# Kernel optimization log

Measured on AMD Instinct MI355X. Metric: run time of the kernel, lower is better.

## Reference

```python
import jax, jax.numpy as jnp
import numpy as np

N_NODES = 50000
N_EDGES = 600000
D = 128


def setup_inputs() -> dict:
    key = jax.random.key(0)
    k = jax.random.split(key, 6)
    x = jax.random.normal(k[0], (N_NODES, D), dtype=jnp.float32)
    edge_src = jax.random.randint(k[1], (N_EDGES,), 0, N_NODES, dtype=jnp.int64 if jax.config.jax_enable_x64 else jnp.int32)
    edge_dst = jax.random.randint(k[2], (N_EDGES,), 0, N_NODES, dtype=jnp.int64 if jax.config.jax_enable_x64 else jnp.int32)
    # message MLP: [h_src ; h_dst] (2D) -> D, update MLP: [h ; agg] (2D) -> D
    scale = 1.0 / np.sqrt(2 * D)
    W1 = jax.random.normal(k[3], (2 * D, D), dtype=jnp.float32) * scale
    b1 = jnp.zeros((D,), dtype=jnp.float32)
    W2 = jax.random.normal(k[4], (2 * D, D), dtype=jnp.float32) * scale
    b2 = jnp.zeros((D,), dtype=jnp.float32)
    return {"x": x, "edge_src": edge_src, "edge_dst": edge_dst,
            "W1": W1, "b1": b1, "W2": W2, "b2": b2}


def reference(x, edge_src, edge_dst, W1, b1, W2, b2):
    # gather endpoint features per edge: [E, 2D]
    pair = jnp.concatenate([x[edge_src], x[edge_dst]], axis=-1)
    # per-edge message MLP: [E, D]
    msg = jax.nn.relu(pair @ W1 + b1)
    # scatter-aggregate (sum) messages into destination nodes: [N, D]
    agg = jax.ops.segment_sum(msg, edge_dst, num_segments=N_NODES)
    # node update MLP with residual: [N, D]
    upd = jax.nn.relu(jnp.concatenate([x, agg], axis=-1) @ W2 + b2)
    return x + upd
```

## Files before the change

kernel.cpp:

```cpp
#include <hip/hip_runtime.h>
#include <stdint.h>


typedef __attribute__((ext_vector_type(8))) short short8;
typedef __attribute__((ext_vector_type(4))) float floatx4;

#define D 128

static __device__ __forceinline__ unsigned short f2bf(float f) {
    union { float f; unsigned int u; } v; v.f = f;
    unsigned int r = (v.u + 0x7fffu + ((v.u >> 16) & 1u)) >> 16;
    return (unsigned short)r;
}
static __device__ __forceinline__ float bflo(unsigned int u) {
    union { unsigned int u; float f; } v; v.u = u << 16; return v.f;
}
static __device__ __forceinline__ float bfhi(unsigned int u) {
    union { unsigned int u; float f; } v; v.u = u & 0xffff0000u; return v.f;
}

__global__ void k_convert_w(const float* __restrict__ W1, const float* __restrict__ W2,
                            unsigned short* __restrict__ w1f, unsigned short* __restrict__ w2f,
                            int* __restrict__ cursor, int N) {
    int gid = blockIdx.x * blockDim.x + threadIdx.x;
    if (gid < N) cursor[gid] = 0;
    if (gid < 32768) {
        int tid = gid;
        int j = tid & 7, lane = (tid >> 3) & 63, ct = (tid >> 9) & 15, kk = tid >> 13;
        int k = kk * 32 + (lane >> 4) * 8 + j;
        int c = ((ct >> 2) << 6) + ((lane & 15) << 2) + (ct & 3);
        float v = (c < 128) ? W1[k * 128 + c] : W1[(128 + k) * 128 + (c - 128)];
        w1f[tid] = f2bf(v);
    } else {
        int tid = gid - 32768;
        int j = tid & 7, lane = (tid >> 3) & 63, ct = (tid >> 9) & 7, kk = tid >> 12;
        int k = kk * 32 + (lane >> 4) * 8 + j;
        int c = ((ct >> 1) << 5) + ((lane & 15) << 1) + (ct & 1);
        w2f[tid] = f2bf(W2[k * 128 + c]);
    }
}

__global__ __launch_bounds__(256) void k_gemm1(
    const float* __restrict__ x,
    const unsigned short* __restrict__ w1f,
    const float* __restrict__ b1,
    unsigned short* __restrict__ xb,
    unsigned short* __restrict__ Ys,
    unsigned short* __restrict__ Yd,
    int N, int nTiles)
{
    const int tid = threadIdx.x, w = tid >> 6, lane = tid & 63;
    const int quad = lane >> 4, col = lane & 15;

    short8 wf[4][4];
#pragma unroll
    for (int kk = 0; kk < 4; kk++)
#pragma unroll
        for (int j = 0; j < 4; j++)
            wf[kk][j] = ((const short8*)w1f)[(kk * 16 + w * 4 + j) * 64 + lane];
    float4 bias = make_float4(0.f, 0.f, 0.f, 0.f);
    if (w >= 2) bias = *(const float4*)(b1 + (w - 2) * 64 + col * 4);
    unsigned short* Yhalf = (w < 2) ? Ys : Yd;
    const int cb = (w & 1) * 64;

    for (int t = blockIdx.x; t < nTiles; t += gridDim.x) {
        const int n0 = t * 16;
        const int nr = n0 + col;
        const float* xrow = x + (long)nr * D;
        floatx4 acc[4];
#pragma unroll
        for (int j = 0; j < 4; j++)
#pragma unroll
            for (int q = 0; q < 4; q++) acc[j][q] = 0.f;
#pragma unroll
        for (int kk = 0; kk < 4; kk++) {
            float4 f0 = *(const float4*)(xrow + kk * 32 + quad * 8);
            float4 f1 = *(const float4*)(xrow + kk * 32 + quad * 8 + 4);
            union { short8 s; unsigned int u[4]; } au;
            asm("v_cvt_pk_bf16_f32 %0, %1, %2" : "=v"(au.u[0]) : "v"(f0.x), "v"(f0.y));
            asm("v_cvt_pk_bf16_f32 %0, %1, %2" : "=v"(au.u[1]) : "v"(f0.z), "v"(f0.w));
            asm("v_cvt_pk_bf16_f32 %0, %1, %2" : "=v"(au.u[2]) : "v"(f1.x), "v"(f1.y));
            asm("v_cvt_pk_bf16_f32 %0, %1, %2" : "=v"(au.u[3]) : "v"(f1.z), "v"(f1.w));
            if (w == 0)
                *(short8*)(xb + (long)nr * D + kk * 32 + quad * 8) = au.s;
#pragma unroll
            for (int j = 0; j < 4; j++)
                acc[j] = __builtin_amdgcn_mfma_f32_16x16x32_bf16(au.s, wf[kk][j], acc[j], 0, 0, 0);
        }
#pragma unroll
        for (int r = 0; r < 4; r++) {
            int n = n0 + quad * 4 + r;
            ushort4 o;
            o.x = f2bf(acc[0][r] + bias.x);
            o.y = f2bf(acc[1][r] + bias.y);
            o.z = f2bf(acc[2][r] + bias.z);
            o.w = f2bf(acc[3][r] + bias.w);
            *(ushort4*)(Yhalf + (long)n * D + cb + col * 4) = o;
        }
    }
}

__global__ void k_hist(const int* __restrict__ dst, int* __restrict__ cnt, int E) {
    int i = blockIdx.x * blockDim.x + threadIdx.x;
    if (i < E) atomicAdd(&cnt[dst[i]], 1);
}

__global__ void k_scanA(const int* __restrict__ cnt, int* __restrict__ rowptr,
                        int* __restrict__ bsum, int N) {
    __shared__ int ws[16];
    int tid = threadIdx.x, i = blockIdx.x * 1024 + tid;
    int lane = tid & 63, wv = tid >> 6;
    int c = (i < N) ? cnt[i] : 0;
    int incl = c;
#pragma unroll
    for (int off = 1; off < 64; off <<= 1) {
        int t = __shfl_up(incl, off, 64);
        if (lane >= off) incl += t;
    }
    if (lane == 63) ws[wv] = incl;
    __syncthreads();
    if (wv == 0) {
        int v = (lane < 16) ? ws[lane] : 0;
        int s = v;
#pragma unroll
        for (int off = 1; off < 16; off <<= 1) {
            int t = __shfl_up(s, off, 64);
            if (lane >= off) s += t;
        }
        if (lane < 16) ws[lane] = s - v;
    }
    __syncthreads();
    if (i < N) rowptr[i] = incl - c + ws[wv];
    if (tid == 1023) bsum[blockIdx.x] = ws[15] + incl;
}

__global__ void k_scanC(int* __restrict__ rowptr, int* __restrict__ cursor,
                        const int* __restrict__ bsum, int N, int E, int nb) {
    __shared__ int off_s;
    int tid = threadIdx.x;
    int chunk = blockIdx.x >> 2;
    if (tid < 64) {
        int v = (tid < chunk && tid < nb) ? bsum[tid] : 0;
#pragma unroll
        for (int off = 32; off; off >>= 1) v += __shfl_down(v, off, 64);
        if (tid == 0) off_s = v;
    }
    __syncthreads();
    int i = blockIdx.x * 256 + tid;
    if (i < N) {
        int r = rowptr[i] + off_s;
        rowptr[i] = r;
        cursor[i] = r;
    }
    if (i == 0) rowptr[N] = E;
}

__global__ void k_scatter(const int* __restrict__ src, const int* __restrict__ dst,
                          int* __restrict__ cursor, int* __restrict__ ssrc, int E) {
    int i = blockIdx.x * blockDim.x + threadIdx.x;
    if (i < E) {
        int p = atomicAdd(&cursor[dst[i]], 1);
        ssrc[p] = src[i];
    }
}

__global__ __launch_bounds__(256) void k_agg(
    const unsigned short* __restrict__ Ys,
    const unsigned short* __restrict__ Yd,
    const int* __restrict__ rowptr,
    const int* __restrict__ ssrc,
    unsigned short* __restrict__ aggb, int N)
{
    int wv = blockIdx.x * 4 + (threadIdx.x >> 6);
    if (wv >= N) return;
    int lane = threadIdx.x & 63;
    int rp0 = rowptr[wv], rp1 = rowptr[wv + 1];
    unsigned int ydu = *(const unsigned int*)(Yd + (long)wv * D + lane * 2);
    float yd0 = bflo(ydu), yd1 = bfhi(ydu);
    float a0 = 0.f, a1 = 0.f;
    const unsigned short* ysl = Ys + lane * 2;
    int e = rp0;
    for (; e + 8 <= rp1; e += 8) {
        int s[8]; unsigned int u[8];
#pragma unroll
        for (int q = 0; q < 8; q++) s[q] = ssrc[e + q];
#pragma unroll
        for (int q = 0; q < 8; q++) u[q] = *(const unsigned int*)(ysl + (long)s[q] * D);
#pragma unroll
        for (int q = 0; q < 8; q++) {
            a0 += fmaxf(bflo(u[q]) + yd0, 0.f);
            a1 += fmaxf(bfhi(u[q]) + yd1, 0.f);
        }
    }
    for (; e + 4 <= rp1; e += 4) {
        int s[4]; unsigned int u[4];
#pragma unroll
        for (int q = 0; q < 4; q++) s[q] = ssrc[e + q];
#pragma unroll
        for (int q = 0; q < 4; q++) u[q] = *(const unsigned int*)(ysl + (long)s[q] * D);
#pragma unroll
        for (int q = 0; q < 4; q++) {
            a0 += fmaxf(bflo(u[q]) + yd0, 0.f);
            a1 += fmaxf(bfhi(u[q]) + yd1, 0.f);
        }
    }
    for (; e < rp1; e++) {
        unsigned int u0 = *(const unsigned int*)(ysl + (long)ssrc[e] * D);
        a0 += fmaxf(bflo(u0) + yd0, 0.f);
        a1 += fmaxf(bfhi(u0) + yd1, 0.f);
    }
    unsigned int o = (unsigned int)f2bf(a0) | ((unsigned int)f2bf(a1) << 16);
    *(unsigned int*)(aggb + (long)wv * D + lane * 2) = o;
}

__global__ __launch_bounds__(256) void k_gemm2(
    const unsigned short* __restrict__ xb,
    const unsigned short* __restrict__ aggb,
    const unsigned short* __restrict__ w2f,
    const float* __restrict__ b2,
    const float* __restrict__ x,
    float* __restrict__ out,
    int N, int nTiles)
{
    const int tid = threadIdx.x, w = tid >> 6, lane = tid & 63;
    const int quad = lane >> 4, col = lane & 15;

    short8 wf[8][2];
#pragma unroll
    for (int kk = 0; kk < 8; kk++)
#pragma unroll
        for (int c = 0; c < 2; c++)
            wf[kk][c] = ((const short8*)w2f)[(kk * 8 + w * 2 + c) * 64 + lane];
    float2 bias = *(const float2*)(b2 + w * 32 + col * 2);

    for (int t = blockIdx.x; t < nTiles; t += gridDim.x) {
        const int n0 = t * 16;
        const int nr = n0 + col;
        floatx4 acc[2];
#pragma unroll
        for (int c = 0; c < 2; c++)
#pragma unroll
            for (int q = 0; q < 4; q++) acc[c][q] = 0.f;
#pragma unroll
        for (int kk = 0; kk < 8; kk++) {
            const unsigned short* base = (kk < 4) ? xb : aggb;
            short8 a = *(const short8*)(base + (long)nr * D + (kk & 3) * 32 + quad * 8);
            acc[0] = __builtin_amdgcn_mfma_f32_16x16x32_bf16(a, wf[kk][0], acc[0], 0, 0, 0);
            acc[1] = __builtin_amdgcn_mfma_f32_16x16x32_bf16(a, wf[kk][1], acc[1], 0, 0, 0);
        }
#pragma unroll
        for (int r = 0; r < 4; r++) {
            int n = n0 + quad * 4 + r;
            long off = (long)n * D + w * 32 + col * 2;
            float2 xr = *(const float2*)(x + off);
            float v0 = fmaxf(acc[0][r] + bias.x, 0.f);
            float v1 = fmaxf(acc[1][r] + bias.y, 0.f);
            *(float2*)(out + off) = make_float2(xr.x + v0, xr.y + v1);
        }
    }
}

extern "C" void kernel_launch(void* const* d_in, const int* in_sizes, int n_in,
                              void* d_out, int out_size, void* d_ws, size_t ws_size,
                              hipStream_t stream)
{
    const float* x   = (const float*)d_in[0];
    const int* esrc  = (const int*)d_in[1];
    const int* edst  = (const int*)d_in[2];
    const float* W1  = (const float*)d_in[3];
    const float* b1  = (const float*)d_in[4];
    const float* W2  = (const float*)d_in[5];
    const float* b2  = (const float*)d_in[6];
    float* out = (float*)d_out;

    const int ND = in_sizes[0];
    const int N  = ND / D;
    const int E  = in_sizes[1];

    char* p = (char*)d_ws;
    auto alloc = [&](size_t bytes) { char* r = p; p += (bytes + 255) & ~(size_t)255; return r; };
    unsigned short* Ys   = (unsigned short*)alloc((size_t)ND * 2);
    unsigned short* Yd   = (unsigned short*)alloc((size_t)ND * 2);
    unsigned short* xb   = (unsigned short*)alloc((size_t)ND * 2);
    unsigned short* aggb = (unsigned short*)alloc((size_t)ND * 2);
    unsigned short* w1f  = (unsigned short*)alloc(32768 * 2);
    unsigned short* w2f  = (unsigned short*)alloc(32768 * 2);
    int* rowptr = (int*)alloc((size_t)(N + 1) * 4);
    int* cursor = (int*)alloc((size_t)N * 4);
    int* bsum   = (int*)alloc(64 * 4);
    int* ssrc   = (int*)alloc((size_t)E * 4);

    const int nTiles = N / 16;
    const int nb = (N + 1023) / 1024;

    k_convert_w<<<256, 256, 0, stream>>>(W1, W2, w1f, w2f, cursor, N);
    k_gemm1<<<1024, 256, 0, stream>>>(x, w1f, b1, xb, Ys, Yd, N, nTiles);
    k_hist<<<(E + 255) / 256, 256, 0, stream>>>(edst, cursor, E);
    k_scanA<<<nb, 1024, 0, stream>>>(cursor, rowptr, bsum, N);
    k_scanC<<<(N + 255) / 256, 256, 0, stream>>>(rowptr, cursor, bsum, N, E, nb);
    k_scatter<<<(E + 255) / 256, 256, 0, stream>>>(esrc, edst, cursor, ssrc, E);
    k_agg<<<(N + 3) / 4, 256, 0, stream>>>(Ys, Yd, rowptr, ssrc, aggb, N);
    k_gemm2<<<1024, 256, 0, stream>>>(xb, aggb, w2f, b2, x, out, N, nTiles);
}
```

Measured before the change: 211.9 us.

## Fuse all pipeline stages into one cooperative persistent kernel with grid syncs

Replaces the eight separate launches (weight conversion, GEMM1, histogram, two scan passes, scatter, aggregation, GEMM2) with one cooperative kernel that separates phases with grid.sync(). It also drops the bf16 copy of x: GEMM2 now reloads fp32 x and converts it in registers. The histogram is fused into the GEMM1 phase, and the scan is reworked to four elements per thread across 256-thread blocks. The aim is to remove per-launch overhead and inter-kernel gaps. The cost is grid-wide barriers, reduced occupancy because the grid is capped by cooperative residency, and the combined register pressure of all phases in one kernel.

Result: slower. 468.5 us (+121.1%).

```diff
diff --git a/kernel.cpp b/kernel.cpp
--- a/kernel.cpp
+++ b/kernel.cpp
@@ -1,5 +1,8 @@
 #include <hip/hip_runtime.h>
+#include <hip/hip_cooperative_groups.h>
 #include <stdint.h>
+
+namespace cg = cooperative_groups;
 
 
 typedef __attribute__((ext_vector_type(8))) short short8;
@@ -19,243 +22,260 @@
     union { unsigned int u; float f; } v; v.u = u & 0xffff0000u; return v.f;
 }
 
-__global__ void k_convert_w(const float* __restrict__ W1, const float* __restrict__ W2,
-                            unsigned short* __restrict__ w1f, unsigned short* __restrict__ w2f,
-                            int* __restrict__ cursor, int N) {
-    int gid = blockIdx.x * blockDim.x + threadIdx.x;
-    if (gid < N) cursor[gid] = 0;
-    if (gid < 32768) {
-        int tid = gid;
-        int j = tid & 7, lane = (tid >> 3) & 63, ct = (tid >> 9) & 15, kk = tid >> 13;
-        int k = kk * 32 + (lane >> 4) * 8 + j;
-        int c = ((ct >> 2) << 6) + ((lane & 15) << 2) + (ct & 3);
-        float v = (c < 128) ? W1[k * 128 + c] : W1[(128 + k) * 128 + (c - 128)];
-        w1f[tid] = f2bf(v);
-    } else {
-        int tid = gid - 32768;
-        int j = tid & 7, lane = (tid >> 3) & 63, ct = (tid >> 9) & 7, kk = tid >> 12;
-        int k = kk * 32 + (lane >> 4) * 8 + j;
-        int c = ((ct >> 1) << 5) + ((lane & 15) << 1) + (ct & 1);
-        w2f[tid] = f2bf(W2[k * 128 + c]);
-    }
-}
-
-__global__ __launch_bounds__(256) void k_gemm1(
+
+__global__ __launch_bounds__(256) void k_mega(
     const float* __restrict__ x,
-    const unsigned short* __restrict__ w1f,
+    const int* __restrict__ esrc,
+    const int* __restrict__ edst,
+    const float* __restrict__ W1,
     const float* __restrict__ b1,
-    unsigned short* __restrict__ xb,
+    const float* __restrict__ W2,
+    const float* __restrict__ b2,
+    float* __restrict__ out,
+    unsigned short* __restrict__ w1f,
+    unsigned short* __restrict__ w2f,
     unsigned short* __restrict__ Ys,
     unsigned short* __restrict__ Yd,
-    int N, int nTiles)
+    unsigned short* __restrict__ aggb,
+    int* __restrict__ cnt,
+    int* __restrict__ rowptr,
+    int* __restrict__ cursor,
+    int* __restrict__ bsum,
+    int* __restrict__ ssrc,
+    int N, int E, int nTiles)
 {
-    const int tid = threadIdx.x, w = tid >> 6, lane = tid & 63;
+    cg::grid_group grid = cg::this_grid();
+    const int G  = gridDim.x;
+    const int GT = G * 256;
+    const int tid = threadIdx.x;
+    const int gid0 = blockIdx.x * 256 + tid;
+    const int w = tid >> 6, lane = tid & 63;
     const int quad = lane >> 4, col = lane & 15;
-
-    short8 wf[4][4];
-#pragma unroll
-    for (int kk = 0; kk < 4; kk++)
-#pragma unroll
-        for (int j = 0; j < 4; j++)
-            wf[kk][j] = ((const short8*)w1f)[(kk * 16 + w * 4 + j) * 64 + lane];
-    float4 bias = make_float4(0.f, 0.f, 0.f, 0.f);
-    if (w >= 2) bias = *(const float4*)(b1 + (w - 2) * 64 + col * 4);
-    unsigned short* Yhalf = (w < 2) ? Ys : Yd;
-    const int cb = (w & 1) * 64;
-
-    for (int t = blockIdx.x; t < nTiles; t += gridDim.x) {
-        const int n0 = t * 16;
-        const int nr = n0 + col;
-        const float* xrow = x + (long)nr * D;
-        floatx4 acc[4];
-#pragma unroll
-        for (int j = 0; j < 4; j++)
-#pragma unroll
-            for (int q = 0; q < 4; q++) acc[j][q] = 0.f;
-#pragma unroll
-        for (int kk = 0; kk < 4; kk++) {
-            float4 f0 = *(const float4*)(xrow + kk * 32 + quad * 8);
-            float4 f1 = *(const float4*)(xrow + kk * 32 + quad * 8 + 4);
-            union { short8 s; unsigned int u[4]; } au;
-            asm("v_cvt_pk_bf16_f32 %0, %1, %2" : "=v"(au.u[0]) : "v"(f0.x), "v"(f0.y));
-            asm("v_cvt_pk_bf16_f32 %0, %1, %2" : "=v"(au.u[1]) : "v"(f0.z), "v"(f0.w));
-            asm("v_cvt_pk_bf16_f32 %0, %1, %2" : "=v"(au.u[2]) : "v"(f1.x), "v"(f1.y));
-            asm("v_cvt_pk_bf16_f32 %0, %1, %2" : "=v"(au.u[3]) : "v"(f1.z), "v"(f1.w));
-            if (w == 0)
-                *(short8*)(xb + (long)nr * D + kk * 32 + quad * 8) = au.s;
+    __shared__ int sh[9];
+
+    for (int i = gid0; i < N; i += GT) cnt[i] = 0;
+    for (int g = gid0; g < 65536; g += GT) {
+        if (g < 32768) {
+            int j = g & 7, l = (g >> 3) & 63, ct = (g >> 9) & 15, kk = g >> 13;
+            int k = kk * 32 + (l >> 4) * 8 + j;
+            int c = ((ct >> 2) << 6) + ((l & 15) << 2) + (ct & 3);
+            float v = (c < 128) ? W1[k * 128 + c] : W1[(128 + k) * 128 + (c - 128)];
+            w1f[g] = f2bf(v);
+        } else {
+            int t2 = g - 32768;
+            int j = t2 & 7, l = (t2 >> 3) & 63, ct = (t2 >> 9) & 7, kk = t2 >> 12;
+            int k = kk * 32 + (l >> 4) * 8 + j;
+            int c = ((ct >> 1) << 5) + ((l & 15) << 1) + (ct & 1);
+            w2f[t2] = f2bf(W2[k * 128 + c]);
+        }
+    }
+    grid.sync();
+
+    {
+        short8 wf[4][4];
+#pragma unroll
+        for (int kk = 0; kk < 4; kk++)
 #pragma unroll
             for (int j = 0; j < 4; j++)
-                acc[j] = __builtin_amdgcn_mfma_f32_16x16x32_bf16(au.s, wf[kk][j], acc[j], 0, 0, 0);
-        }
-#pragma unroll
-        for (int r = 0; r < 4; r++) {
-            int n = n0 + quad * 4 + r;
-            ushort4 o;
-            o.x = f2bf(acc[0][r] + bias.x);
-            o.y = f2bf(acc[1][r] + bias.y);
-            o.z = f2bf(acc[2][r] + bias.z);
-            o.w = f2bf(acc[3][r] + bias.w);
-            *(ushort4*)(Yhalf + (long)n * D + cb + col * 4) = o;
-        }
-    }
-}
-
-__global__ void k_hist(const int* __restrict__ dst, int* __restrict__ cnt, int E) {
-    int i = blockIdx.x * blockDim.x + threadIdx.x;
-    if (i < E) atomicAdd(&cnt[dst[i]], 1);
-}
-
-__global__ void k_scanA(const int* __restrict__ cnt, int* __restrict__ rowptr,
-                        int* __restrict__ bsum, int N) {
-    __shared__ int ws[16];
-    int tid = threadIdx.x, i = blockIdx.x * 1024 + tid;
-    int lane = tid & 63, wv = tid >> 6;
-    int c = (i < N) ? cnt[i] : 0;
-    int incl = c;
-#pragma unroll
-    for (int off = 1; off < 64; off <<= 1) {
-        int t = __shfl_up(incl, off, 64);
-        if (lane >= off) incl += t;
-    }
-    if (lane == 63) ws[wv] = incl;
-    __syncthreads();
-    if (wv == 0) {
-        int v = (lane < 16) ? ws[lane] : 0;
-        int s = v;
-#pragma unroll
-        for (int off = 1; off < 16; off <<= 1) {
-            int t = __shfl_up(s, off, 64);
-            if (lane >= off) s += t;
-        }
-        if (lane < 16) ws[lane] = s - v;
-    }
-    __syncthreads();
-    if (i < N) rowptr[i] = incl - c + ws[wv];
-    if (tid == 1023) bsum[blockIdx.x] = ws[15] + incl;
-}
-
-__global__ void k_scanC(int* __restrict__ rowptr, int* __restrict__ cursor,
-                        const int* __restrict__ bsum, int N, int E, int nb) {
-    __shared__ int off_s;
-    int tid = threadIdx.x;
-    int chunk = blockIdx.x >> 2;
-    if (tid < 64) {
-        int v = (tid < chunk && tid < nb) ? bsum[tid] : 0;
-#pragma unroll
-        for (int off = 32; off; off >>= 1) v += __shfl_down(v, off, 64);
-        if (tid == 0) off_s = v;
-    }
-    __syncthreads();
-    int i = blockIdx.x * 256 + tid;
-    if (i < N) {
-        int r = rowptr[i] + off_s;
-        rowptr[i] = r;
-        cursor[i] = r;
-    }
-    if (i == 0) rowptr[N] = E;
-}
-
-__global__ void k_scatter(const int* __restrict__ src, const int* __restrict__ dst,
-                          int* __restrict__ cursor, int* __restrict__ ssrc, int E) {
-    int i = blockIdx.x * blockDim.x + threadIdx.x;
-    if (i < E) {
-        int p = atomicAdd(&cursor[dst[i]], 1);
-        ssrc[p] = src[i];
-    }
-}
-
-__global__ __launch_bounds__(256) void k_agg(
-    const unsigned short* __restrict__ Ys,
-    const unsigned short* __restrict__ Yd,
-    const int* __restrict__ rowptr,
-    const int* __restrict__ ssrc,
-    unsigned short* __restrict__ aggb, int N)
-{
-    int wv = blockIdx.x * 4 + (threadIdx.x >> 6);
-    if (wv >= N) return;
-    int lane = threadIdx.x & 63;
-    int rp0 = rowptr[wv], rp1 = rowptr[wv + 1];
-    unsigned int ydu = *(const unsigned int*)(Yd + (long)wv * D + lane * 2);
-    float yd0 = bflo(ydu), yd1 = bfhi(ydu);
-    float a0 = 0.f, a1 = 0.f;
-    const unsigned short* ysl = Ys + lane * 2;
-    int e = rp0;
-    for (; e + 8 <= rp1; e += 8) {
-        int s[8]; unsigned int u[8];
-#pragma unroll
-        for (int q = 0; q < 8; q++) s[q] = ssrc[e + q];
-#pragma unroll
-        for (int q = 0; q < 8; q++) u[q] = *(const unsigned int*)(ysl + (long)s[q] * D);
-#pragma unroll
-        for (int q = 0; q < 8; q++) {
-            a0 += fmaxf(bflo(u[q]) + yd0, 0.f);
-            a1 += fmaxf(bfhi(u[q]) + yd1, 0.f);
-        }
-    }
-    for (; e + 4 <= rp1; e += 4) {
-        int s[4]; unsigned int u[4];
-#pragma unroll
-        for (int q = 0; q < 4; q++) s[q] = ssrc[e + q];
-#pragma unroll
-        for (int q = 0; q < 4; q++) u[q] = *(const unsigned int*)(ysl + (long)s[q] * D);
-#pragma unroll
-        for (int q = 0; q < 4; q++) {
-            a0 += fmaxf(bflo(u[q]) + yd0, 0.f);
-            a1 += fmaxf(bfhi(u[q]) + yd1, 0.f);
-        }
-    }
-    for (; e < rp1; e++) {
-        unsigned int u0 = *(const unsigned int*)(ysl + (long)ssrc[e] * D);
-        a0 += fmaxf(bflo(u0) + yd0, 0.f);
-        a1 += fmaxf(bfhi(u0) + yd1, 0.f);
-    }
-    unsigned int o = (unsigned int)f2bf(a0) | ((unsigned int)f2bf(a1) << 16);
-    *(unsigned int*)(aggb + (long)wv * D + lane * 2) = o;
-}
-
-__global__ __launch_bounds__(256) void k_gemm2(
-    const unsigned short* __restrict__ xb,
-    const unsigned short* __restrict__ aggb,
-    const unsigned short* __restrict__ w2f,
-    const float* __restrict__ b2,
-    const float* __restrict__ x,
-    float* __restrict__ out,
-    int N, int nTiles)
-{
-    const int tid = threadIdx.x, w = tid >> 6, lane = tid & 63;
-    const int quad = lane >> 4, col = lane & 15;
-
-    short8 wf[8][2];
-#pragma unroll
-    for (int kk = 0; kk < 8; kk++)
-#pragma unroll
-        for (int c = 0; c < 2; c++)
-            wf[kk][c] = ((const short8*)w2f)[(kk * 8 + w * 2 + c) * 64 + lane];
-    float2 bias = *(const float2*)(b2 + w * 32 + col * 2);
-
-    for (int t = blockIdx.x; t < nTiles; t += gridDim.x) {
-        const int n0 = t * 16;
-        const int nr = n0 + col;
-        floatx4 acc[2];
-#pragma unroll
-        for (int c = 0; c < 2; c++)
-#pragma unroll
-            for (int q = 0; q < 4; q++) acc[c][q] = 0.f;
-#pragma unroll
-        for (int kk = 0; kk < 8; kk++) {
-            const unsigned short* base = (kk < 4) ? xb : aggb;
-            short8 a = *(const short8*)(base + (long)nr * D + (kk & 3) * 32 + quad * 8);
-            acc[0] = __builtin_amdgcn_mfma_f32_16x16x32_bf16(a, wf[kk][0], acc[0], 0, 0, 0);
-            acc[1] = __builtin_amdgcn_mfma_f32_16x16x32_bf16(a, wf[kk][1], acc[1], 0, 0, 0);
-        }
-#pragma unroll
-        for (int r = 0; r < 4; r++) {
-            int n = n0 + quad * 4 + r;
-            long off = (long)n * D + w * 32 + col * 2;
-            float2 xr = *(const float2*)(x + off);
-            float v0 = fmaxf(acc[0][r] + bias.x, 0.f);
-            float v1 = fmaxf(acc[1][r] + bias.y, 0.f);
-            *(float2*)(out + off) = make_float2(xr.x + v0, xr.y + v1);
+                wf[kk][j] = ((const short8*)w1f)[(kk * 16 + w * 4 + j) * 64 + lane];
+        float4 bias = make_float4(0.f, 0.f, 0.f, 0.f);
+        if (w >= 2) bias = *(const float4*)(b1 + (w - 2) * 64 + col * 4);
+        unsigned short* Yhalf = (w < 2) ? Ys : Yd;
+        const int cb = (w & 1) * 64;
+
+        for (int t = blockIdx.x; t < nTiles; t += G) {
+            const int n0 = t * 16;
+            const int nr = n0 + col;
+            const float* xrow = x + (long)nr * D;
+            floatx4 acc[4];
+#pragma unroll
+            for (int j = 0; j < 4; j++)
+#pragma unroll
+                for (int q = 0; q < 4; q++) acc[j][q] = 0.f;
+#pragma unroll
+            for (int kk = 0; kk < 4; kk++) {
+                float4 f0 = *(const float4*)(xrow + kk * 32 + quad * 8);
+                float4 f1 = *(const float4*)(xrow + kk * 32 + quad * 8 + 4);
+                union { short8 s; unsigned int u[4]; } au;
+                asm("v_cvt_pk_bf16_f32 %0, %1, %2" : "=v"(au.u[0]) : "v"(f0.x), "v"(f0.y));
+                asm("v_cvt_pk_bf16_f32 %0, %1, %2" : "=v"(au.u[1]) : "v"(f0.z), "v"(f0.w));
+                asm("v_cvt_pk_bf16_f32 %0, %1, %2" : "=v"(au.u[2]) : "v"(f1.x), "v"(f1.y));
+                asm("v_cvt_pk_bf16_f32 %0, %1, %2" : "=v"(au.u[3]) : "v"(f1.z), "v"(f1.w));
+#pragma unroll
+                for (int j = 0; j < 4; j++)
+                    acc[j] = __builtin_amdgcn_mfma_f32_16x16x32_bf16(au.s, wf[kk][j], acc[j], 0, 0, 0);
+            }
+#pragma unroll
+            for (int r = 0; r < 4; r++) {
+                int n = n0 + quad * 4 + r;
+                ushort4 o;
+                o.x = f2bf(acc[0][r] + bias.x);
+                o.y = f2bf(acc[1][r] + bias.y);
+                o.z = f2bf(acc[2][r] + bias.z);
+                o.w = f2bf(acc[3][r] + bias.w);
+                *(ushort4*)(Yhalf + (long)n * D + cb + col * 4) = o;
+            }
+        }
+    }
+    for (int i = gid0; i < E; i += GT) atomicAdd(&cnt[edst[i]], 1);
+    grid.sync();
+
+    {
+        const int nbChunks = (N + 1023) >> 10;
+        for (int b = blockIdx.x; b < nbChunks; b += G) {
+            int i0 = (b << 10) + tid * 4;
+            int v0 = 0, v1 = 0, v2 = 0, v3 = 0;
+            if (i0 + 3 < N) {
+                int4 c4 = *(const int4*)(cnt + i0);
+                v0 = c4.x; v1 = c4.y; v2 = c4.z; v3 = c4.w;
+            } else {
+                if (i0     < N) v0 = cnt[i0];
+                if (i0 + 1 < N) v1 = cnt[i0 + 1];
+                if (i0 + 2 < N) v2 = cnt[i0 + 2];
+                if (i0 + 3 < N) v3 = cnt[i0 + 3];
+            }
+            int s1 = v0 + v1, s2 = s1 + v2, S = s2 + v3;
+            int incl = S;
+#pragma unroll
+            for (int off = 1; off < 64; off <<= 1) {
+                int tt = __shfl_up(incl, off, 64);
+                if (lane >= off) incl += tt;
+            }
+            if (lane == 63) sh[w] = incl;
+            __syncthreads();
+            if (tid == 0) {
+                int a0 = sh[0], a1 = sh[1], a2 = sh[2], a3 = sh[3];
+                sh[0] = 0; sh[1] = a0; sh[2] = a0 + a1; sh[3] = a0 + a1 + a2;
+                sh[4] = a0 + a1 + a2 + a3;
+            }
+            __syncthreads();
+            int texcl = incl - S + sh[w];
+            if (i0 + 3 < N) {
+                *(int4*)(rowptr + i0) = make_int4(texcl, texcl + v0, texcl + s1, texcl + s2);
+            } else {
+                if (i0     < N) rowptr[i0]     = texcl;
+                if (i0 + 1 < N) rowptr[i0 + 1] = texcl + v0;
+                if (i0 + 2 < N) rowptr[i0 + 2] = texcl + s1;
+                if (i0 + 3 < N) rowptr[i0 + 3] = texcl + s2;
+            }
+            if (tid == 0) bsum[b] = sh[4];
+            __syncthreads();
+        }
+    }
+    grid.sync();
+
+    for (long ib = (long)blockIdx.x * 256; ib < N; ib += GT) {
+        int chunk = (int)(ib >> 10);
+        if (tid < 64) {
+            int v = (tid < chunk) ? bsum[tid] : 0;
+#pragma unroll
+            for (int off = 32; off; off >>= 1) v += __shfl_down(v, off, 64);
+            if (tid == 0) sh[8] = v;
+        }
+        __syncthreads();
+        int i = (int)ib + tid;
+        if (i < N) {
+            int r = rowptr[i] + sh[8];
+            rowptr[i] = r;
+            cursor[i] = r;
+        }
+        __syncthreads();
+    }
+    if (gid0 == 0) rowptr[N] = E;
+    grid.sync();
+
+    for (int i = gid0; i < E; i += GT) {
+        int p = atomicAdd(&cursor[edst[i]], 1);
+        ssrc[p] = esrc[i];
+    }
+    grid.sync();
+
+    for (int wv = blockIdx.x * 4 + w; wv < N; wv += G * 4) {
+        int rp0 = rowptr[wv], rp1 = rowptr[wv + 1];
+        unsigned int ydu = *(const unsigned int*)(Yd + (long)wv * D + lane * 2);
+        float yd0 = bflo(ydu), yd1 = bfhi(ydu);
+        float a0 = 0.f, a1 = 0.f;
+        const unsigned short* ysl = Ys + lane * 2;
+        int e = rp0;
+        for (; e + 8 <= rp1; e += 8) {
+            int s[8]; unsigned int u[8];
+#pragma unroll
+            for (int q = 0; q < 8; q++) s[q] = ssrc[e + q];
+#pragma unroll
+            for (int q = 0; q < 8; q++) u[q] = *(const unsigned int*)(ysl + (long)s[q] * D);
+#pragma unroll
+            for (int q = 0; q < 8; q++) {
+                a0 += fmaxf(bflo(u[q]) + yd0, 0.f);
+                a1 += fmaxf(bfhi(u[q]) + yd1, 0.f);
+            }
+        }
+        for (; e + 4 <= rp1; e += 4) {
+            int s[4]; unsigned int u[4];
+#pragma unroll
+            for (int q = 0; q < 4; q++) s[q] = ssrc[e + q];
+#pragma unroll
+            for (int q = 0; q < 4; q++) u[q] = *(const unsigned int*)(ysl + (long)s[q] * D);
+#pragma unroll
+            for (int q = 0; q < 4; q++) {
+                a0 += fmaxf(bflo(u[q]) + yd0, 0.f);
+                a1 += fmaxf(bfhi(u[q]) + yd1, 0.f);
+            }
+        }
+        for (; e < rp1; e++) {
+            unsigned int u0 = *(const unsigned int*)(ysl + (long)ssrc[e] * D);
+            a0 += fmaxf(bflo(u0) + yd0, 0.f);
+            a1 += fmaxf(bfhi(u0) + yd1, 0.f);
+        }
+        unsigned int o = (unsigned int)f2bf(a0) | ((unsigned int)f2bf(a1) << 16);
+        *(unsigned int*)(aggb + (long)wv * D + lane * 2) = o;
+    }
+    grid.sync();
+
+    {
+        short8 wf2[8][2];
+#pragma unroll
+        for (int kk = 0; kk < 8; kk++)
+#pragma unroll
+            for (int c = 0; c < 2; c++)
+                wf2[kk][c] = ((const short8*)w2f)[(kk * 8 + w * 2 + c) * 64 + lane];
+        float2 bias2 = *(const float2*)(b2 + w * 32 + col * 2);
+
+        for (int t = blockIdx.x; t < nTiles; t += G) {
+            const int n0 = t * 16;
+            const int nr = n0 + col;
+            const float* xrow = x + (long)nr * D;
+            floatx4 acc[2];
+#pragma unroll
+            for (int c = 0; c < 2; c++)
+#pragma unroll
+                for (int q = 0; q < 4; q++) acc[c][q] = 0.f;
+#pragma unroll
+            for (int kk = 0; kk < 4; kk++) {
+                float4 f0 = *(const float4*)(xrow + kk * 32 + quad * 8);
+                float4 f1 = *(const float4*)(xrow + kk * 32 + quad * 8 + 4);
+                union { short8 s; unsigned int u[4]; } au;
+                asm("v_cvt_pk_bf16_f32 %0, %1, %2" : "=v"(au.u[0]) : "v"(f0.x), "v"(f0.y));
+                asm("v_cvt_pk_bf16_f32 %0, %1, %2" : "=v"(au.u[1]) : "v"(f0.z), "v"(f0.w));
+                asm("v_cvt_pk_bf16_f32 %0, %1, %2" : "=v"(au.u[2]) : "v"(f1.x), "v"(f1.y));
+                asm("v_cvt_pk_bf16_f32 %0, %1, %2" : "=v"(au.u[3]) : "v"(f1.z), "v"(f1.w));
+                acc[0] = __builtin_amdgcn_mfma_f32_16x16x32_bf16(au.s, wf2[kk][0], acc[0], 0, 0, 0);
+                acc[1] = __builtin_amdgcn_mfma_f32_16x16x32_bf16(au.s, wf2[kk][1], acc[1], 0, 0, 0);
+            }
+#pragma unroll
+            for (int kk = 4; kk < 8; kk++) {
+                short8 a = *(const short8*)(aggb + (long)nr * D + (kk - 4) * 32 + quad * 8);
+                acc[0] = __builtin_amdgcn_mfma_f32_16x16x32_bf16(a, wf2[kk][0], acc[0], 0, 0, 0);
+                acc[1] = __builtin_amdgcn_mfma_f32_16x16x32_bf16(a, wf2[kk][1], acc[1], 0, 0, 0);
+            }
+#pragma unroll
+            for (int r = 0; r < 4; r++) {
+                int n = n0 + quad * 4 + r;
+                long off = (long)n * D + w * 32 + col * 2;
+                float2 xr = *(const float2*)(x + off);
+                float v0 = fmaxf(acc[0][r] + bias2.x, 0.f);
+                float v1 = fmaxf(acc[1][r] + bias2.y, 0.f);
+                *(float2*)(out + off) = make_float2(xr.x + v0, xr.y + v1);
+            }
         }
     }
 }
@@ -274,31 +294,44 @@
     float* out = (float*)d_out;
 
     const int ND = in_sizes[0];
-    const int N  = ND / D;
-    const int E  = in_sizes[1];
+    int N = ND / D;
+    int E = in_sizes[1];
 
     char* p = (char*)d_ws;
     auto alloc = [&](size_t bytes) { char* r = p; p += (bytes + 255) & ~(size_t)255; return r; };
     unsigned short* Ys   = (unsigned short*)alloc((size_t)ND * 2);
     unsigned short* Yd   = (unsigned short*)alloc((size_t)ND * 2);
-    unsigned short* xb   = (unsigned short*)alloc((size_t)ND * 2);
     unsigned short* aggb = (unsigned short*)alloc((size_t)ND * 2);
     unsigned short* w1f  = (unsigned short*)alloc(32768 * 2);
     unsigned short* w2f  = (unsigned short*)alloc(32768 * 2);
     int* rowptr = (int*)alloc((size_t)(N + 1) * 4);
     int* cursor = (int*)alloc((size_t)N * 4);
+    int* cnt    = (int*)alloc((size_t)N * 4);
     int* bsum   = (int*)alloc(64 * 4);
     int* ssrc   = (int*)alloc((size_t)E * 4);
 
-    const int nTiles = N / 16;
-    const int nb = (N + 1023) / 1024;
-
-    k_convert_w<<<256, 256, 0, stream>>>(W1, W2, w1f, w2f, cursor, N);
-    k_gemm1<<<1024, 256, 0, stream>>>(x, w1f, b1, xb, Ys, Yd, N, nTiles);
-    k_hist<<<(E + 255) / 256, 256, 0, stream>>>(edst, cursor, E);
-    k_scanA<<<nb, 1024, 0, stream>>>(cursor, rowptr, bsum, N);
-    k_scanC<<<(N + 255) / 256, 256, 0, stream>>>(rowptr, cursor, bsum, N, E, nb);
-    k_scatter<<<(E + 255) / 256, 256, 0, stream>>>(esrc, edst, cursor, ssrc, E);
-    k_agg<<<(N + 3) / 4, 256, 0, stream>>>(Ys, Yd, rowptr, ssrc, aggb, N);
-    k_gemm2<<<1024, 256, 0, stream>>>(xb, aggb, w2f, b2, x, out, N, nTiles);
-}
+    int nTiles = N / 16;
+
+    static int G = 0;
+    if (G == 0) {
+        int nb = 0;
+        hipError_t e1 = hipOccupancyMaxActiveBlocksPerMultiprocessor(&nb, k_mega, 256, 0);
+        int cus = 256;
+        hipDeviceProp_t prop;
+        if (hipGetDeviceProperties(&prop, 0) == hipSuccess && prop.multiProcessorCount > 0)
+            cus = prop.multiProcessorCount;
+        long g = (e1 == hipSuccess && nb > 0) ? (long)nb * cus : 256;
+        if (g > 1536) g = 1536;
+        if (g < 64)  g = 64;
+        G = (int)g;
+    }
+
+    void* args[] = {
+        (void*)&x, (void*)&esrc, (void*)&edst, (void*)&W1, (void*)&b1,
+        (void*)&W2, (void*)&b2, (void*)&out, (void*)&w1f, (void*)&w2f,
+        (void*)&Ys, (void*)&Yd, (void*)&aggb, (void*)&cnt, (void*)&rowptr,
+        (void*)&cursor, (void*)&bsum, (void*)&ssrc,
+        (void*)&N, (void*)&E, (void*)&nTiles
+    };
+    hipLaunchCooperativeKernel(k_mega, dim3(G), dim3(256), args, 0, stream);
+}
```
